# Kernel optimization log

Hardware: AMD Instinct MI355X
Metric: run time of the kernel (lower is better)

## Reference

```python
import jax, jax.numpy as jnp
import numpy as np

B, IN_DIM, OUT_DIM, DEGREE = 4096, 1024, 1024, 4
LN_EPS = 1e-5


def setup_inputs() -> dict:
    key = jax.random.key(0)
    k_x, k_c = jax.random.split(key)
    x = jax.random.normal(k_x, (B, IN_DIM), dtype=jnp.float32)
    # xavier_normal_ on tensor of shape (in, out, deg+1): fan_in/fan_out from
    # torch convention: fan_in = out*(deg+1)? torch computes fan_in=size(1)*receptive,
    # for 3D tensor fan_in = shape[1]*shape[2], fan_out = shape[0]*shape[2].
    fan_in = OUT_DIM * (DEGREE + 1)
    fan_out = IN_DIM * (DEGREE + 1)
    std = float(np.sqrt(2.0 / (fan_in + fan_out)))
    cheby_coeffs = jax.random.normal(k_c, (IN_DIM, OUT_DIM, DEGREE + 1), dtype=jnp.float32) * std
    ln_weight = jnp.ones((IN_DIM,), dtype=jnp.float32)
    ln_bias = jnp.zeros((IN_DIM,), dtype=jnp.float32)
    return {"x": x, "cheby_coeffs": cheby_coeffs, "ln_weight": ln_weight, "ln_bias": ln_bias}


def _layer_norm(x, w, b):
    mu = jnp.mean(x, axis=-1, keepdims=True)
    var = jnp.mean(jnp.square(x - mu), axis=-1, keepdims=True)
    return (x - mu) * jax.lax.rsqrt(var + LN_EPS) * w + b


def reference(x, cheby_coeffs, ln_weight, ln_bias):
    h = jnp.tanh(_layer_norm(x, ln_weight, ln_bias))  # [B, I]
    # Chebyshev recurrence T0=1, T1=h, T_{n}=2h*T_{n-1}-T_{n-2}
    cheby = [jnp.ones_like(h), h]
    for _ in range(2, DEGREE + 1):
        cheby.append(2.0 * h * cheby[-1] - cheby[-2])
    stacked = jnp.stack(cheby, axis=-1)  # [B, I, D+1]
    y = jnp.einsum('bid,iod->bo', stacked, cheby_coeffs)
    return jax.nn.silu(y)
```

## Files before the change

### kernel.cpp

```cpp
#include <hip/hip_runtime.h>
#include <cstdint>
#include <cstddef>

#define BATCH 4096
#define IDIM 1024
#define ODIM 1024
#define KDIM 4096

typedef __attribute__((ext_vector_type(4))) int i32x4;
typedef __attribute__((ext_vector_type(16))) int i32x16;

#define CS_INV 1514.7f
#define DEQ_SCALE (6.602e-4f / 127.0f)

__device__ __forceinline__ char q8(float v, float s) {
  int i = __float2int_rn(v * s);
  i = max(-127, min(127, i));
  return (char)i;
}

__device__ __forceinline__ void load_lds16(const void* g, void* l) {
  __builtin_amdgcn_global_load_lds(
      (const __attribute__((address_space(1))) void*)g,
      (__attribute__((address_space(3))) void*)l, 16, 0, 0);
}

__global__ __launch_bounds__(256) void prep(
    const float* __restrict__ x, const float* __restrict__ lnw,
    const float* __restrict__ lnb, const float* __restrict__ C,
    char* __restrict__ A, char* __restrict__ Bq,
    float* __restrict__ bias) {
  __shared__ __align__(16) char smq[5 * 64 * 64];
  __shared__ float smf[64 * 64];
  int bid = blockIdx.x;
  int t = threadIdx.x;

  if (bid < BATCH) {
    float* rs = smf;
    float* rq = smf + 4;
    const float4 v = ((const float4*)(x + (size_t)bid * IDIM))[t];
    float s  = v.x + v.y + v.z + v.w;
    float s2 = v.x * v.x + v.y * v.y + v.z * v.z + v.w * v.w;
#pragma unroll
    for (int off = 32; off > 0; off >>= 1) {
      s  += __shfl_down(s, off);
      s2 += __shfl_down(s2, off);
    }
    int lane = t & 63, wv = t >> 6;
    if (lane == 0) { rs[wv] = s; rq[wv] = s2; }
    __syncthreads();
    float S1 = rs[0] + rs[1] + rs[2] + rs[3];
    float S2 = rq[0] + rq[1] + rq[2] + rq[3];
    float mean = S1 * (1.0f / IDIM);
    float var  = S2 * (1.0f / IDIM) - mean * mean;
    float rstd = rsqrtf(var + 1e-5f);

    const float4 w4 = ((const float4*)lnw)[t];
    const float4 b4 = ((const float4*)lnb)[t];
    float xs[4]  = {v.x, v.y, v.z, v.w};
    float ws4[4] = {w4.x, w4.y, w4.z, w4.w};
    float bs4[4] = {b4.x, b4.y, b4.z, b4.w};

    char q1[4], q2[4], q3[4], q4[4];
#pragma unroll
    for (int j = 0; j < 4; j++) {
      float h  = tanhf((xs[j] - mean) * rstd * ws4[j] + bs4[j]);
      float T2 = 2.0f * h * h - 1.0f;
      float T3 = 2.0f * h * T2 - h;
      float T4 = 2.0f * h * T3 - T2;
      q1[j] = q8(h, 127.f); q2[j] = q8(T2, 127.f);
      q3[j] = q8(T3, 127.f); q4[j] = q8(T4, 127.f);
    }
    size_t base = (size_t)bid * KDIM;
    *(uint32_t*)(A + base + 0 * IDIM + t * 4) = *(uint32_t*)q1;
    *(uint32_t*)(A + base + 1 * IDIM + t * 4) = *(uint32_t*)q2;
    *(uint32_t*)(A + base + 2 * IDIM + t * 4) = *(uint32_t*)q3;
    *(uint32_t*)(A + base + 3 * IDIM + t * 4) = *(uint32_t*)q4;
  } else {
    int cb = bid - BATCH;
    int i0 = (cb & 15) * 64, o0 = (cb >> 4) * 64;
#pragma unroll
    for (int r = 0; r < 20; r++) {
      int idx = r * 256 + t;
      int ii  = idx / 80;
      int c4  = idx - ii * 80;
      const float4 f = *(const float4*)(C + ((size_t)(i0 + ii) * ODIM + o0) * 5 + c4 * 4);
      float vals[4] = {f.x, f.y, f.z, f.w};
#pragma unroll
      for (int j = 0; j < 4; j++) {
        int p  = c4 * 4 + j;
        int oo = p / 5, d = p - oo * 5;
        if (d == 0) smf[oo * 64 + ii] = vals[j];
        else        smq[p * 64 + ((ii + 4 * p) & 63)] = q8(vals[j], CS_INV);
      }
    }
    __syncthreads();
#pragma unroll
    for (int r = 0; r < 16; r++) {
      int idx = r * 256 + t;
      int seg = idx >> 4, l16 = idx & 15;
      int oo = seg >> 2, d2 = seg & 3;
      int p = oo * 5 + d2 + 1;
      char4 u = *(const char4*)&smq[p * 64 + 4 * ((l16 + p) & 15)];
      *(char4*)(Bq + (size_t)(o0 + oo) * KDIM + d2 * IDIM + i0 + l16 * 4) = u;
    }
    if (t < 64) {
      float s = 0.f;
#pragma unroll
      for (int k = 0; k < 64; k++) s += smf[t * 64 + ((k + t) & 63)];
      atomicAdd(&bias[o0 + t], s);
    }
  }
}

#define BM 128
#define BN 128
#define BKB 128
#define NIT (KDIM / BKB)
#define BUFB (BM * BKB)

#define WAIT_BAR(N)                                                          \
  do {                                                                       \
    asm volatile("s_waitcnt vmcnt(" #N ")" ::: "memory");                    \
    __builtin_amdgcn_s_barrier();                                            \
  } while (0)

__global__ __launch_bounds__(512, 2) void gemm_fused(
    const char* __restrict__ A,
    const char* __restrict__ Bq,
    const float* __restrict__ bias,
    float* __restrict__ out) {
  __shared__ char As[4][BUFB];
  __shared__ char Bs[4][BUFB];
  int t = threadIdx.x;
  int lane = t & 63, w = t >> 6;

  int bid = blockIdx.x;
  int swz = ((bid & 7) << 5) | (bid >> 3);
  int m0 = (swz >> 3) * BM;
  int n0 = (swz & 7) * BN;

  i32x16 acc[2];
#pragma unroll
  for (int i = 0; i < 2; i++)
#pragma unroll
    for (int r = 0; r < 16; r++) acc[i][r] = 0;

  int wm = (w >> 2) * 64;
  int wn = (w & 3) * 32;

  int sr = lane >> 3;
  int sc = ((lane & 7) ^ sr) * 16;
  const char* ag[2]; char* al[2];
  const char* bg[2]; char* bl[2];
#pragma unroll
  for (int q = 0; q < 2; q++) {
    int row = w * 16 + q * 8;
    ag[q] = A  + (size_t)(m0 + row + sr) * KDIM + sc;
    al[q] = &As[0][row * BKB];
    bg[q] = Bq + (size_t)(n0 + row + sr) * KDIM + sc;
    bl[q] = &Bs[0][row * BKB];
  }

  int l31 = lane & 31, hb = lane >> 5, x7 = lane & 7;
  int arow0 = (wm + l31) * BKB;
  int brow0 = (wn + l31) * BKB;

#define ISSUE(buf, kk0)                                                      \
  do {                                                                       \
    int _k = (kk0);                                                          \
    _Pragma("unroll")                                                        \
    for (int q = 0; q < 2; q++) load_lds16(ag[q] + _k, al[q] + (buf) * BUFB); \
    _Pragma("unroll")                                                        \
    for (int q = 0; q < 2; q++) load_lds16(bg[q] + _k, bl[q] + (buf) * BUFB); \
  } while (0)

#define COMPUTE(buf)                                                         \
  do {                                                                       \
    const char* asb = &As[buf][0];                                           \
    const char* bsb = &Bs[buf][0];                                           \
    _Pragma("unroll")                                                        \
    for (int ks = 0; ks < 4; ks++) {                                         \
      int co = ((2 * ks + hb) ^ x7) * 16;                                    \
      i32x4 af[2], bf;                                                       \
      _Pragma("unroll")                                                      \
      for (int i = 0; i < 2; i++)                                            \
        af[i]  = *(const i32x4*)(asb + arow0 + i * 32 * BKB + co);           \
      bf = *(const i32x4*)(bsb + brow0 + co);                                \
      __builtin_amdgcn_s_setprio(1);                                         \
      _Pragma("unroll")                                                      \
      for (int i = 0; i < 2; i++)                                            \
        acc[i] = __builtin_amdgcn_mfma_i32_32x32x32_i8(                      \
            af[i], bf, acc[i], 0, 0, 0);                                     \
      __builtin_amdgcn_s_setprio(0);                                         \
    }                                                                        \
  } while (0)

  ISSUE(0, 0);
  ISSUE(1, 1 * BKB);
  ISSUE(2, 2 * BKB);

#pragma unroll 1
  for (int jj = 0; jj < 28; jj += 4) {
    WAIT_BAR(8); ISSUE(3, (jj + 3) * BKB); COMPUTE(0);
    WAIT_BAR(8); ISSUE(0, (jj + 4) * BKB); COMPUTE(1);
    WAIT_BAR(8); ISSUE(1, (jj + 5) * BKB); COMPUTE(2);
    WAIT_BAR(8); ISSUE(2, (jj + 6) * BKB); COMPUTE(3);
  }
  WAIT_BAR(8); ISSUE(3, 31 * BKB); COMPUTE(0);
  WAIT_BAR(8); COMPUTE(1);
  WAIT_BAR(4); COMPUTE(2);
  WAIT_BAR(0); COMPUTE(3);

  {
    int col = n0 + wn + l31;
    float bcol = bias[col];
#pragma unroll
    for (int ii = 0; ii < 2; ii++) {
      int rbase = m0 + wm + ii * 32 + 4 * hb;
#pragma unroll
      for (int reg = 0; reg < 16; reg++) {
        int row = rbase + (reg & 3) + 8 * (reg >> 2);
        float y = (float)acc[ii][reg] * DEQ_SCALE + bcol;
        out[(size_t)row * ODIM + col] = y / (1.0f + __expf(-y));
      }
    }
  }
}

extern "C" void kernel_launch(void* const* d_in, const int* in_sizes, int n_in,
                              void* d_out, int out_size, void* d_ws, size_t ws_size,
                              hipStream_t stream) {
  const float* x    = (const float*)d_in[0];
  const float* coef = (const float*)d_in[1];
  const float* lnw  = (const float*)d_in[2];
  const float* lnb  = (const float*)d_in[3];
  float* out = (float*)d_out;

  char* ws = (char*)d_ws;
  char* A    = ws;
  char* Bq   = ws + (size_t)BATCH * KDIM;
  float* bias = (float*)(Bq + (size_t)ODIM * KDIM);

  hipMemsetAsync(bias, 0, ODIM * sizeof(float), stream);
  prep<<<BATCH + 256, 256, 0, stream>>>(x, lnw, lnb, coef, A, Bq, bias);
  gemm_fused<<<dim3(256), 512, 0, stream>>>(A, Bq, bias, out);
}
```

Measured before the change: 127.7 us.

## Load B fragments directly into registers, drop bias atomics and memset

The GEMM now loads B operand fragments from global memory straight into double-buffered registers instead of staging them through LDS, which halves LDS usage and removes the B LDS reads. The prep kernel writes per-block partial bias sums into a buffer that the GEMM epilogue reduces, replacing atomicAdd and the separate memset launch. Launch bounds drop to one block per SM. Global register loads of B are less coalesced and their latency must be hidden by a shorter prefetch distance, and the wait counts were retuned to match.

```diff
diff --git a/kernel.cpp b/kernel.cpp
--- a/kernel.cpp
+++ b/kernel.cpp
@@ -29,7 +29,7 @@
     const float* __restrict__ x, const float* __restrict__ lnw,
     const float* __restrict__ lnb, const float* __restrict__ C,
     char* __restrict__ A, char* __restrict__ Bq,
-    float* __restrict__ bias) {
+    float* __restrict__ bias_part) {
   __shared__ __align__(16) char smq[5 * 64 * 64];
   __shared__ float smf[64 * 64];
   int bid = blockIdx.x;
@@ -108,7 +108,7 @@
       float s = 0.f;
 #pragma unroll
       for (int k = 0; k < 64; k++) s += smf[t * 64 + ((k + t) & 63)];
-      atomicAdd(&bias[o0 + t], s);
+      bias_part[(cb & 15) * ODIM + o0 + t] = s;
     }
   }
 }
@@ -125,13 +125,12 @@
     __builtin_amdgcn_s_barrier();                                            \
   } while (0)
 
-__global__ __launch_bounds__(512, 2) void gemm_fused(
+__global__ __launch_bounds__(512, 1) void gemm_fused(
     const char* __restrict__ A,
     const char* __restrict__ Bq,
-    const float* __restrict__ bias,
+    const float* __restrict__ bias_part,
     float* __restrict__ out) {
   __shared__ char As[4][BUFB];
-  __shared__ char Bs[4][BUFB];
   int t = threadIdx.x;
   int lane = t & 63, w = t >> 6;
 
@@ -152,69 +151,76 @@
   int sr = lane >> 3;
   int sc = ((lane & 7) ^ sr) * 16;
   const char* ag[2]; char* al[2];
-  const char* bg[2]; char* bl[2];
 #pragma unroll
   for (int q = 0; q < 2; q++) {
     int row = w * 16 + q * 8;
-    ag[q] = A  + (size_t)(m0 + row + sr) * KDIM + sc;
+    ag[q] = A + (size_t)(m0 + row + sr) * KDIM + sc;
     al[q] = &As[0][row * BKB];
-    bg[q] = Bq + (size_t)(n0 + row + sr) * KDIM + sc;
-    bl[q] = &Bs[0][row * BKB];
   }
 
   int l31 = lane & 31, hb = lane >> 5, x7 = lane & 7;
   int arow0 = (wm + l31) * BKB;
-  int brow0 = (wn + l31) * BKB;
-
-#define ISSUE(buf, kk0)                                                      \
-  do {                                                                       \
-    int _k = (kk0);                                                          \
+
+  const char* bgp = Bq + (size_t)(n0 + wn + l31) * KDIM + hb * 16;
+  i32x4 bfA[4], bfB[4];
+
+#define ISSUE(buf, cj)                                                       \
+  do {                                                                       \
+    int _k = (cj) * BKB;                                                     \
     _Pragma("unroll")                                                        \
     for (int q = 0; q < 2; q++) load_lds16(ag[q] + _k, al[q] + (buf) * BUFB); \
+  } while (0)
+
+#define B_LOAD(arr, cj)                                                      \
+  do {                                                                       \
+    int _k = (cj) * BKB;                                                     \
     _Pragma("unroll")                                                        \
-    for (int q = 0; q < 2; q++) load_lds16(bg[q] + _k, bl[q] + (buf) * BUFB); \
-  } while (0)
-
-#define COMPUTE(buf)                                                         \
+    for (int ks = 0; ks < 4; ks++)                                           \
+      arr[ks] = *(const i32x4*)(bgp + _k + ks * 32);                         \
+  } while (0)
+
+#define COMPUTE(buf, arr)                                                    \
   do {                                                                       \
     const char* asb = &As[buf][0];                                           \
-    const char* bsb = &Bs[buf][0];                                           \
     _Pragma("unroll")                                                        \
     for (int ks = 0; ks < 4; ks++) {                                         \
       int co = ((2 * ks + hb) ^ x7) * 16;                                    \
-      i32x4 af[2], bf;                                                       \
+      i32x4 af[2];                                                           \
       _Pragma("unroll")                                                      \
       for (int i = 0; i < 2; i++)                                            \
-        af[i]  = *(const i32x4*)(asb + arow0 + i * 32 * BKB + co);           \
-      bf = *(const i32x4*)(bsb + brow0 + co);                                \
+        af[i] = *(const i32x4*)(asb + arow0 + i * 32 * BKB + co);            \
       __builtin_amdgcn_s_setprio(1);                                         \
       _Pragma("unroll")                                                      \
       for (int i = 0; i < 2; i++)                                            \
         acc[i] = __builtin_amdgcn_mfma_i32_32x32x32_i8(                      \
-            af[i], bf, acc[i], 0, 0, 0);                                     \
+            af[i], arr[ks], acc[i], 0, 0, 0);                                \
       __builtin_amdgcn_s_setprio(0);                                         \
     }                                                                        \
   } while (0)
 
   ISSUE(0, 0);
-  ISSUE(1, 1 * BKB);
-  ISSUE(2, 2 * BKB);
+  ISSUE(1, 1);
+  ISSUE(2, 2);
+  asm volatile("" ::: "memory");
+  B_LOAD(bfA, 0);
 
 #pragma unroll 1
-  for (int jj = 0; jj < 28; jj += 4) {
-    WAIT_BAR(8); ISSUE(3, (jj + 3) * BKB); COMPUTE(0);
-    WAIT_BAR(8); ISSUE(0, (jj + 4) * BKB); COMPUTE(1);
-    WAIT_BAR(8); ISSUE(1, (jj + 5) * BKB); COMPUTE(2);
-    WAIT_BAR(8); ISSUE(2, (jj + 6) * BKB); COMPUTE(3);
-  }
-  WAIT_BAR(8); ISSUE(3, 31 * BKB); COMPUTE(0);
-  WAIT_BAR(8); COMPUTE(1);
-  WAIT_BAR(4); COMPUTE(2);
-  WAIT_BAR(0); COMPUTE(3);
+  for (int j = 0; j < 28; j += 4) {
+    WAIT_BAR(6); B_LOAD(bfB, j + 1); ISSUE(3, j + 3); COMPUTE(0, bfA);
+    WAIT_BAR(6); B_LOAD(bfA, j + 2); ISSUE(0, j + 4); COMPUTE(1, bfB);
+    WAIT_BAR(6); B_LOAD(bfB, j + 3); ISSUE(1, j + 5); COMPUTE(2, bfA);
+    WAIT_BAR(6); B_LOAD(bfA, j + 4); ISSUE(2, j + 6); COMPUTE(3, bfB);
+  }
+  WAIT_BAR(6); B_LOAD(bfB, 29); ISSUE(3, 31); COMPUTE(0, bfA);
+  WAIT_BAR(6); B_LOAD(bfA, 30); COMPUTE(1, bfB);
+  WAIT_BAR(6); B_LOAD(bfB, 31); COMPUTE(2, bfA);
+  WAIT_BAR(4); COMPUTE(3, bfB);
 
   {
     int col = n0 + wn + l31;
-    float bcol = bias[col];
+    float bcol = 0.f;
+#pragma unroll
+    for (int ib = 0; ib < 16; ib++) bcol += bias_part[ib * ODIM + col];
 #pragma unroll
     for (int ii = 0; ii < 2; ii++) {
       int rbase = m0 + wm + ii * 32 + 4 * hb;
@@ -240,9 +246,8 @@
   char* ws = (char*)d_ws;
   char* A    = ws;
   char* Bq   = ws + (size_t)BATCH * KDIM;
-  float* bias = (float*)(Bq + (size_t)ODIM * KDIM);
-
-  hipMemsetAsync(bias, 0, ODIM * sizeof(float), stream);
-  prep<<<BATCH + 256, 256, 0, stream>>>(x, lnw, lnb, coef, A, Bq, bias);
-  gemm_fused<<<dim3(256), 512, 0, stream>>>(A, Bq, bias, out);
-}
+  float* bias_part = (float*)(Bq + (size_t)ODIM * KDIM);
+
+  prep<<<BATCH + 256, 256, 0, stream>>>(x, lnw, lnb, coef, A, Bq, bias_part);
+  gemm_fused<<<dim3(256), 512, 0, stream>>>(A, Bq, bias_part, out);
+}
```

Result: slower. 142.2 us (+11.4%).

## Drop bias memset via partial-bias buffer, one-wave-per-row layernorm, fast tanh

Applied to the files above, without the earlier changes.

Removes the hipMemsetAsync and the atomicAdd bias accumulation. Each coefficient block now writes its own partial bias row, and the GEMM epilogue sums the 16 partials. The layernorm prep is reorganised so each wave handles one row, with shuffle-xor reductions and no block barrier, cutting the LN block count from 4096 to 1024. It also swaps tanhf for an exp-based approximation and relaxes the GEMM launch bound from 2 to 1 blocks per CU, which risks lower occupancy and adds 16 loads per thread in the epilogue.

```diff
diff --git a/kernel.cpp b/kernel.cpp
--- a/kernel.cpp
+++ b/kernel.cpp
@@ -19,65 +19,83 @@
   return (char)i;
 }
 
+__device__ __forceinline__ float tanh_fast(float x) {
+  float xc = fminf(fmaxf(x, -20.f), 20.f);
+  float t = __expf(2.0f * xc);
+  return 1.0f - 2.0f / (t + 1.0f);
+}
+
 __device__ __forceinline__ void load_lds16(const void* g, void* l) {
   __builtin_amdgcn_global_load_lds(
       (const __attribute__((address_space(1))) void*)g,
       (__attribute__((address_space(3))) void*)l, 16, 0, 0);
 }
 
+#define LNBLK 1024
+
 __global__ __launch_bounds__(256) void prep(
     const float* __restrict__ x, const float* __restrict__ lnw,
     const float* __restrict__ lnb, const float* __restrict__ C,
     char* __restrict__ A, char* __restrict__ Bq,
-    float* __restrict__ bias) {
-  __shared__ __align__(16) char smq[5 * 64 * 64];
-  __shared__ float smf[64 * 64];
+    float* __restrict__ bias_part) {
   int bid = blockIdx.x;
   int t = threadIdx.x;
 
-  if (bid < BATCH) {
-    float* rs = smf;
-    float* rq = smf + 4;
-    const float4 v = ((const float4*)(x + (size_t)bid * IDIM))[t];
-    float s  = v.x + v.y + v.z + v.w;
-    float s2 = v.x * v.x + v.y * v.y + v.z * v.z + v.w * v.w;
+  if (bid < LNBLK) {
+    int lane = t & 63, wv = t >> 6;
+    int row = bid * 4 + wv;
+    const float* xr = x + (size_t)row * IDIM;
+
+    float4 v[4], w4[4], b4[4];
+#pragma unroll
+    for (int j = 0; j < 4; j++) {
+      int off = j * 64 + lane;
+      v[j]  = ((const float4*)xr)[off];
+      w4[j] = ((const float4*)lnw)[off];
+      b4[j] = ((const float4*)lnb)[off];
+    }
+    float s = 0.f, s2 = 0.f;
+#pragma unroll
+    for (int j = 0; j < 4; j++) {
+      s  += v[j].x + v[j].y + v[j].z + v[j].w;
+      s2 += v[j].x * v[j].x + v[j].y * v[j].y +
+            v[j].z * v[j].z + v[j].w * v[j].w;
+    }
 #pragma unroll
     for (int off = 32; off > 0; off >>= 1) {
-      s  += __shfl_down(s, off);
-      s2 += __shfl_down(s2, off);
-    }
-    int lane = t & 63, wv = t >> 6;
-    if (lane == 0) { rs[wv] = s; rq[wv] = s2; }
-    __syncthreads();
-    float S1 = rs[0] + rs[1] + rs[2] + rs[3];
-    float S2 = rq[0] + rq[1] + rq[2] + rq[3];
-    float mean = S1 * (1.0f / IDIM);
-    float var  = S2 * (1.0f / IDIM) - mean * mean;
+      s  += __shfl_xor(s, off);
+      s2 += __shfl_xor(s2, off);
+    }
+    float mean = s * (1.0f / IDIM);
+    float var  = s2 * (1.0f / IDIM) - mean * mean;
     float rstd = rsqrtf(var + 1e-5f);
 
-    const float4 w4 = ((const float4*)lnw)[t];
-    const float4 b4 = ((const float4*)lnb)[t];
-    float xs[4]  = {v.x, v.y, v.z, v.w};
-    float ws4[4] = {w4.x, w4.y, w4.z, w4.w};
-    float bs4[4] = {b4.x, b4.y, b4.z, b4.w};
-
-    char q1[4], q2[4], q3[4], q4[4];
+    size_t base = (size_t)row * KDIM;
 #pragma unroll
     for (int j = 0; j < 4; j++) {
-      float h  = tanhf((xs[j] - mean) * rstd * ws4[j] + bs4[j]);
-      float T2 = 2.0f * h * h - 1.0f;
-      float T3 = 2.0f * h * T2 - h;
-      float T4 = 2.0f * h * T3 - T2;
-      q1[j] = q8(h, 127.f); q2[j] = q8(T2, 127.f);
-      q3[j] = q8(T3, 127.f); q4[j] = q8(T4, 127.f);
-    }
-    size_t base = (size_t)bid * KDIM;
-    *(uint32_t*)(A + base + 0 * IDIM + t * 4) = *(uint32_t*)q1;
-    *(uint32_t*)(A + base + 1 * IDIM + t * 4) = *(uint32_t*)q2;
-    *(uint32_t*)(A + base + 2 * IDIM + t * 4) = *(uint32_t*)q3;
-    *(uint32_t*)(A + base + 3 * IDIM + t * 4) = *(uint32_t*)q4;
+      float xs[4] = {v[j].x, v[j].y, v[j].z, v[j].w};
+      float ws[4] = {w4[j].x, w4[j].y, w4[j].z, w4[j].w};
+      float bs[4] = {b4[j].x, b4[j].y, b4[j].z, b4[j].w};
+      char q1[4], q2[4], q3[4], q4[4];
+#pragma unroll
+      for (int k = 0; k < 4; k++) {
+        float h  = tanh_fast((xs[k] - mean) * rstd * ws[k] + bs[k]);
+        float T2 = 2.0f * h * h - 1.0f;
+        float T3 = 2.0f * h * T2 - h;
+        float T4 = 2.0f * h * T3 - T2;
+        q1[k] = q8(h, 127.f); q2[k] = q8(T2, 127.f);
+        q3[k] = q8(T3, 127.f); q4[k] = q8(T4, 127.f);
+      }
+      int col = j * 256 + lane * 4;
+      *(uint32_t*)(A + base + 0 * IDIM + col) = *(uint32_t*)q1;
+      *(uint32_t*)(A + base + 1 * IDIM + col) = *(uint32_t*)q2;
+      *(uint32_t*)(A + base + 2 * IDIM + col) = *(uint32_t*)q3;
+      *(uint32_t*)(A + base + 3 * IDIM + col) = *(uint32_t*)q4;
+    }
   } else {
-    int cb = bid - BATCH;
+    __shared__ __align__(16) char smq[5 * 64 * 64];
+    __shared__ float smf[64 * 64];
+    int cb = bid - LNBLK;
     int i0 = (cb & 15) * 64, o0 = (cb >> 4) * 64;
 #pragma unroll
     for (int r = 0; r < 20; r++) {
@@ -108,7 +126,7 @@
       float s = 0.f;
 #pragma unroll
       for (int k = 0; k < 64; k++) s += smf[t * 64 + ((k + t) & 63)];
-      atomicAdd(&bias[o0 + t], s);
+      bias_part[(cb & 15) * ODIM + o0 + t] = s;
     }
   }
 }
@@ -125,10 +143,10 @@
     __builtin_amdgcn_s_barrier();                                            \
   } while (0)
 
-__global__ __launch_bounds__(512, 2) void gemm_fused(
+__global__ __launch_bounds__(512, 1) void gemm_fused(
     const char* __restrict__ A,
     const char* __restrict__ Bq,
-    const float* __restrict__ bias,
+    const float* __restrict__ bias_part,
     float* __restrict__ out) {
   __shared__ char As[4][BUFB];
   __shared__ char Bs[4][BUFB];
@@ -214,7 +232,9 @@
 
   {
     int col = n0 + wn + l31;
-    float bcol = bias[col];
+    float bcol = 0.f;
+#pragma unroll
+    for (int ib = 0; ib < 16; ib++) bcol += bias_part[ib * ODIM + col];
 #pragma unroll
     for (int ii = 0; ii < 2; ii++) {
       int rbase = m0 + wm + ii * 32 + 4 * hb;
@@ -240,9 +260,8 @@
   char* ws = (char*)d_ws;
   char* A    = ws;
   char* Bq   = ws + (size_t)BATCH * KDIM;
-  float* bias = (float*)(Bq + (size_t)ODIM * KDIM);
-
-  hipMemsetAsync(bias, 0, ODIM * sizeof(float), stream);
-  prep<<<BATCH + 256, 256, 0, stream>>>(x, lnw, lnb, coef, A, Bq, bias);
-  gemm_fused<<<dim3(256), 512, 0, stream>>>(A, Bq, bias, out);
-}
+  float* bias_part = (float*)(Bq + (size_t)ODIM * KDIM);
+
+  prep<<<LNBLK + 256, 256, 0, stream>>>(x, lnw, lnb, coef, A, Bq, bias_part);
+  gemm_fused<<<dim3(256), 512, 0, stream>>>(A, Bq, bias_part, out);
+}
```

Measured after the change: 126.8 us. No clear change (-0.7%).
